# Kernel tuning notes

Measured on AMD Instinct MI355X. Metric: run time of the kernel, lower is better.

## Reference

```python
import jax, jax.numpy as jnp
import numpy as np

N_NODES = 100000
N_EDGES = 1600000
D = 128
NUM_LAYERS = 2
EPS = 1e-5


def setup_inputs() -> dict:
    key = jax.random.key(0)
    ks = jax.random.split(key, 8)
    s = 1.0 / np.sqrt(D)
    x = jax.random.normal(ks[0], (N_NODES, D), dtype=jnp.float32)
    edge_index = jax.random.randint(ks[1], (2, N_EDGES), 0, N_NODES, dtype=jnp.int64)
    W1 = jax.random.uniform(ks[2], (D, D), jnp.float32, -s, s)
    b1 = jnp.zeros((D,), jnp.float32)
    W2 = jax.random.uniform(ks[3], (D, D), jnp.float32, -s, s)
    b2 = jnp.zeros((D,), jnp.float32)
    inner = (NUM_LAYERS + 1) * D
    bn_gamma = jnp.ones((inner,), jnp.float32)
    bn_beta = jnp.zeros((inner,), jnp.float32)
    so = 1.0 / np.sqrt(inner)
    Wo = jax.random.uniform(ks[4], (inner, D), jnp.float32, -so, so)
    bo = jax.random.uniform(ks[5], (D,), jnp.float32, -so, so)
    return dict(x=x, edge_index=edge_index, W1=W1, b1=b1, W2=W2, b2=b2,
                bn_gamma=bn_gamma, bn_beta=bn_beta, Wo=Wo, bo=bo)


def gcn_conv(x, src, dst, W, b, n_nodes):
    """PyG GCNConv: symmetric norm with added self-loops, linear then aggregate."""
    h = x @ W  # [N, D]
    deg = jax.ops.segment_sum(jnp.ones_like(src, dtype=h.dtype), dst,
                              num_segments=n_nodes) + 1.0  # +1 self-loop
    dinv = jax.lax.rsqrt(deg)  # deg >= 1 so finite
    norm = dinv[src] * dinv[dst]  # [E]
    msg = h[src] * norm[:, None]  # gather: memory-bound
    agg = jax.ops.segment_sum(msg, dst, num_segments=n_nodes)
    agg = agg + h * (dinv * dinv)[:, None]  # self-loop message
    return agg + b


def reference(x, edge_index, W1, b1, W2, b2, bn_gamma, bn_beta, Wo, bo):
    src, dst = edge_index[0], edge_index[1]
    n = x.shape[0]
    x_cat = [x]
    h = jax.nn.relu(gcn_conv(x, src, dst, W1, b1, n))
    x_cat.append(h)
    h = jax.nn.relu(gcn_conv(h, src, dst, W2, b2, n))
    x_cat.append(h)
    xc = jnp.concatenate(x_cat, axis=-1)  # [N, 3D]
    # BatchNorm1d (training forward: batch statistics, biased variance)
    mu = jnp.mean(xc, axis=0)
    var = jnp.mean(jnp.square(xc - mu), axis=0)
    xn = (xc - mu) * jax.lax.rsqrt(var + EPS) * bn_gamma + bn_beta
    return xn @ Wo + bo  # [N, D]
```

## Files before the change

### kernel.cpp

```cpp
#include <hip/hip_runtime.h>
#include <hip/hip_bf16.h>

#define DD 128
#define NBLK 256
#define MAXBUK 1024
#define CAP2 12288

typedef __attribute__((ext_vector_type(8))) short bf16x8;
typedef __attribute__((ext_vector_type(4))) float f32x4;
typedef unsigned int uint32;

__device__ __forceinline__ unsigned short f2b(float f) {
  __hip_bfloat16 h = __float2bfloat16(f);
  unsigned short u;
  __builtin_memcpy(&u, &h, 2);
  return u;
}
__device__ __forceinline__ float b2f_lo(uint32 v) { return __uint_as_float(v << 16); }
__device__ __forceinline__ float b2f_hi(uint32 v) { return __uint_as_float(v & 0xffff0000u); }

__device__ __forceinline__ void acc8(float* acc, uint4 h, float w) {
  acc[0] = fmaf(w, b2f_lo(h.x), acc[0]);
  acc[1] = fmaf(w, b2f_hi(h.x), acc[1]);
  acc[2] = fmaf(w, b2f_lo(h.y), acc[2]);
  acc[3] = fmaf(w, b2f_hi(h.y), acc[3]);
  acc[4] = fmaf(w, b2f_lo(h.z), acc[4]);
  acc[5] = fmaf(w, b2f_hi(h.z), acc[5]);
  acc[6] = fmaf(w, b2f_lo(h.w), acc[6]);
  acc[7] = fmaf(w, b2f_hi(h.w), acc[7]);
}

__device__ __forceinline__ bool detect_i64(const int* e, int E) {
  int lane = threadIdx.x & 63;
  int samples = E < 64 ? E : 64;
  int v = (lane < samples) ? e[2 * lane + 1] : 0;
  return __ballot(v != 0) == 0ULL;
}

__global__ __launch_bounds__(256) void k_hist(const void* __restrict__ eptr, int E,
                                              int* __restrict__ histT, int nbuk) {
  __shared__ int hist[MAXBUK];
  int t = threadIdx.x, blk = blockIdx.x;
  bool f = detect_i64((const int*)eptr, E);
  for (int b = t; b < nbuk; b += 256) hist[b] = 0;
  __syncthreads();
  int chunk = (E + NBLK - 1) / NBLK;
  int i0 = blk * chunk, i1 = min(E, i0 + chunk);
  for (int i = i0 + t; i < i1; i += 256) {
    int dst = f ? (int)((const long long*)eptr)[E + i] : ((const int*)eptr)[E + i];
    atomicAdd(&hist[dst >> 8], 1);
  }
  __syncthreads();
  for (int b = t; b < nbuk; b += 256) histT[b * NBLK + blk] = hist[b];
}

__global__ __launch_bounds__(1024) void k_bktscan(const int* __restrict__ histT,
                                                  int* __restrict__ offs,
                                                  int* __restrict__ bucketBase,
                                                  int nbuk, int E) {
  __shared__ int tot[MAXBUK];
  int t = threadIdx.x, lane = t & 63, wv = t >> 6;
  for (int b = t; b < MAXBUK; b += 1024) tot[b] = 0;
  __syncthreads();
  for (int b = wv; b < nbuk; b += 16) {
    const int4 vv = *(const int4*)(histT + b * NBLK + lane * 4);
    int lsum = vv.x + vv.y + vv.z + vv.w;
    int s = lsum;
#pragma unroll
    for (int o = 1; o < 64; o <<= 1) {
      int u = __shfl_up(s, o);
      if (lane >= o) s += u;
    }
    if (lane == 63) tot[b] = s;
  }
  __syncthreads();
  for (int o = 1; o < MAXBUK; o <<= 1) {
    int u = (t >= o) ? tot[t - o] : 0;
    __syncthreads();
    tot[t] += u;
    __syncthreads();
  }
  for (int b = wv; b < nbuk; b += 16) {
    int idx = b * NBLK + lane * 4;
    const int4 vv = *(const int4*)(histT + idx);
    int lsum = vv.x + vv.y + vv.z + vv.w;
    int s = lsum;
#pragma unroll
    for (int o = 1; o < 64; o <<= 1) {
      int u = __shfl_up(s, o);
      if (lane >= o) s += u;
    }
    int tb = __shfl(s, 63);
    int bbase = tot[b] - tb;
    int excl = bbase + s - lsum;
    offs[idx] = excl;
    offs[idx + 1] = excl + vv.x;
    offs[idx + 2] = excl + vv.x + vv.y;
    offs[idx + 3] = excl + vv.x + vv.y + vv.z;
    if (lane == 0) bucketBase[b] = bbase;
  }
  if (t == 0) bucketBase[nbuk] = E;
}

__global__ __launch_bounds__(256) void k_place(const void* __restrict__ eptr, int E,
                                               const int* __restrict__ offs,
                                               int* __restrict__ ebuk, int nbuk) {
  __shared__ int cur[MAXBUK];
  int t = threadIdx.x, blk = blockIdx.x;
  bool f = detect_i64((const int*)eptr, E);
  for (int b = t; b < nbuk; b += 256) cur[b] = offs[b * NBLK + blk];
  __syncthreads();
  int chunk = (E + NBLK - 1) / NBLK;
  int i0 = blk * chunk, i1 = min(E, i0 + chunk);
  for (int i = i0 + t; i < i1; i += 256) {
    int src, dst;
    if (f) {
      src = (int)((const long long*)eptr)[i];
      dst = (int)((const long long*)eptr)[E + i];
    } else {
      src = ((const int*)eptr)[i];
      dst = ((const int*)eptr)[E + i];
    }
    int pos = atomicAdd(&cur[dst >> 8], 1);
    ebuk[pos] = (src << 8) | (dst & 255);
  }
}

__global__ __launch_bounds__(256) void k_bsort2(const int* __restrict__ ebuk,
                                                const int* __restrict__ bucketBase,
                                                int* __restrict__ rp, float* __restrict__ dinv,
                                                int* __restrict__ csrc, int n) {
  __shared__ int cnt[256];
  __shared__ int wss[4];
  __shared__ int outb[CAP2];
  int b = blockIdx.x, t = threadIdx.x, lane = t & 63, wv = t >> 6;
  int v0 = b << 8;
  int v1 = min(v0 + 256, n);
  int nn = v1 - v0;
  int base = bucketBase[b];
  int total = bucketBase[b + 1] - base;
  cnt[t] = 0;
  __syncthreads();
  for (int i = t; i < total; i += 256) atomicAdd(&cnt[ebuk[base + i] & 255], 1);
  __syncthreads();
  int v = cnt[t];
  int incl = v;
#pragma unroll
  for (int o = 1; o < 64; o <<= 1) {
    int u = __shfl_up(incl, o);
    if (lane >= o) incl += u;
  }
  if (lane == 63) wss[wv] = incl;
  __syncthreads();
  int woff = 0;
  for (int k = 0; k < wv; ++k) woff += wss[k];
  int excl = woff + incl - v;
  if (t < nn) {
    rp[v0 + t] = base + excl;
    dinv[v0 + t] = rsqrtf((float)v + 1.0f);
  }
  if (t == 255) rp[v1] = base + excl + v;
  __syncthreads();
  cnt[t] = excl;
  __syncthreads();
  if (total <= CAP2) {
    for (int i = t; i < total; i += 256) {
      int e = ebuk[base + i];
      int slot = atomicAdd(&cnt[e & 255], 1);
      outb[slot] = e >> 8;
    }
    __syncthreads();
    for (int i = t; i < total; i += 256) csrc[base + i] = outb[i];
  } else {
    for (int i = t; i < total; i += 256) {
      int e = ebuk[base + i];
      int slot = atomicAdd(&cnt[e & 255], 1);
      csrc[base + slot] = e >> 8;
    }
  }
}

__global__ __launch_bounds__(256) void k_cvtw(const float4* __restrict__ x,
                                              ushort4* __restrict__ xb, int n4,
                                              float* __restrict__ part,
                                              const float* __restrict__ W1,
                                              const float* __restrict__ W2,
                                              unsigned short* __restrict__ wimg) {
  __shared__ float sh[256][8];
  int t = threadIdx.x;
  int bid = blockIdx.x;
  if (bid >= 1024) {
    int i = (bid - 1024) * 256 + t;
    if (i < 32768) {
      int wsel = i >> 14;
      int j = i & 16383;
      int k = j >> 7, col = j & 127;
      float v = (wsel ? W2 : W1)[j];
      int chunk = (k >> 3) ^ (col & 7);
      wimg[wsel * 16384 + col * 128 + chunk * 8 + (k & 7)] = f2b(v);
    }
    return;
  }
  float s[4] = {0, 0, 0, 0}, q[4] = {0, 0, 0, 0};
  for (int i = bid * 256 + t; i < n4; i += 1024 * 256) {
    float4 a = x[i];
    ushort4 o;
    o.x = f2b(a.x); o.y = f2b(a.y); o.z = f2b(a.z); o.w = f2b(a.w);
    xb[i] = o;
    s[0] += a.x; s[1] += a.y; s[2] += a.z; s[3] += a.w;
    q[0] = fmaf(a.x, a.x, q[0]); q[1] = fmaf(a.y, a.y, q[1]);
    q[2] = fmaf(a.z, a.z, q[2]); q[3] = fmaf(a.w, a.w, q[3]);
  }
#pragma unroll
  for (int j = 0; j < 4; ++j) { sh[t][j] = s[j]; sh[t][4 + j] = q[j]; }
  __syncthreads();
  if (t < 32) {
#pragma unroll
    for (int g = 1; g < 8; ++g)
#pragma unroll
      for (int j = 0; j < 4; ++j) {
        s[j] += sh[g * 32 + t][j];
        q[j] += sh[g * 32 + t][4 + j];
      }
    float* pp = part + (size_t)(bid & 63) * 768;
#pragma unroll
    for (int j = 0; j < 4; ++j) {
      atomicAdd(&pp[(t * 4 + j) * 2], s[j]);
      atomicAdd(&pp[(t * 4 + j) * 2 + 1], q[j]);
    }
  }
}

__global__ __launch_bounds__(256) void k_gemm(const unsigned short* __restrict__ Ab,
                                              const unsigned short* __restrict__ Wimg,
                                              const float* __restrict__ dinv,
                                              unsigned short* __restrict__ H, int n) {
  __shared__ __align__(16) unsigned short Wl[16384];
  int t = threadIdx.x, lane = t & 63, w = t >> 6;
#pragma unroll
  for (int i = t; i < 2048; i += 256) ((int4*)Wl)[i] = ((const int4*)Wimg)[i];
  __syncthreads();
  int rowBase = blockIdx.x * 128 + w * 32;
  int r16 = lane & 15, half = lane >> 4;
  f32x4 acc[2][8];
#pragma unroll
  for (int m = 0; m < 2; ++m)
#pragma unroll
    for (int nn = 0; nn < 8; ++nn) acc[m][nn] = (f32x4){0.f, 0.f, 0.f, 0.f};
#pragma unroll
  for (int ks = 0; ks < 4; ++ks) {
    bf16x8 a[2];
#pragma unroll
    for (int m = 0; m < 2; ++m) {
      int r = rowBase + m * 16 + r16;
      if (r >= n) r = n - 1;
      a[m] = *(const bf16x8*)(Ab + (size_t)r * DD + ks * 32 + half * 8);
    }
#pragma unroll
    for (int nn = 0; nn < 8; ++nn) {
      int col = nn * 16 + r16;
      int chunk = (ks * 4 + half) ^ (col & 7);
      bf16x8 b = *(const bf16x8*)(Wl + col * 128 + chunk * 8);
      acc[0][nn] = __builtin_amdgcn_mfma_f32_16x16x32_bf16(a[0], b, acc[0][nn], 0, 0, 0);
      acc[1][nn] = __builtin_amdgcn_mfma_f32_16x16x32_bf16(a[1], b, acc[1][nn], 0, 0, 0);
    }
  }
#pragma unroll
  for (int m = 0; m < 2; ++m) {
    int rb = rowBase + m * 16 + half * 4;
    float dv[4];
#pragma unroll
    for (int i = 0; i < 4; ++i) dv[i] = (rb + i < n) ? dinv[rb + i] : 0.f;
#pragma unroll
    for (int nn = 0; nn < 8; ++nn) {
      int col = nn * 16 + r16;
#pragma unroll
      for (int i = 0; i < 4; ++i) {
        int r = rb + i;
        if (r < n) H[(size_t)r * DD + col] = f2b(acc[m][nn][i] * dv[i]);
      }
    }
  }
}

__global__ __launch_bounds__(256) void k_agg(const unsigned short* __restrict__ hs,
                                             const float* __restrict__ dinv,
                                             const float* __restrict__ b,
                                             const int* __restrict__ rp,
                                             const int* __restrict__ csrc,
                                             unsigned short* __restrict__ y, int n,
                                             float* __restrict__ part, int cb) {
  __shared__ float sh_s[8][128];
  __shared__ float sh_q[8][128];
  int wid = threadIdx.x >> 6, lane = threadIdx.x & 63;
  int eidx = lane >> 4;
  int seg = lane & 15;
  int vA = blockIdx.x * 8 + wid;
  int vB = vA + 4;
  bool okA = vA < n, okB = vB < n;
  int a0 = 0, b0 = 0, a1 = 0, b1 = 0;
  if (okA) { a0 = rp[vA]; b0 = rp[vA + 1]; }
  if (okB) { a1 = rp[vB]; b1 = rp[vB + 1]; }
  const uint4* H4 = (const uint4*)hs;
  uint4 selfA = okA ? H4[(size_t)vA * 16 + seg] : make_uint4(0, 0, 0, 0);
  uint4 selfB = okB ? H4[(size_t)vB * 16 + seg] : make_uint4(0, 0, 0, 0);
  float accA[8], accB[8];
#pragma unroll
  for (int j = 0; j < 8; ++j) { accA[j] = 0.f; accB[j] = 0.f; }
  int ebA = a0, ebB = a1;
  while (ebA < b0 || ebB < b1) {
    int ecA = b0 - ebA; ecA = ecA < 0 ? 0 : (ecA > 64 ? 64 : ecA);
    int ecB = b1 - ebB; ecB = ecB < 0 ? 0 : (ecB > 64 ? 64 : ecB);
    int ulA = (ebA + lane < b0) ? csrc[ebA + lane] : 0;
    int ulB = (ebB + lane < b1) ? csrc[ebB + lane] : 0;
    int iters = ecA > ecB ? ecA : ecB;
    for (int cc = 0; cc < iters; cc += 16) {
      int uA0 = __shfl(ulA, cc + eidx), uA1 = __shfl(ulA, cc + 4 + eidx);
      int uA2 = __shfl(ulA, cc + 8 + eidx), uA3 = __shfl(ulA, cc + 12 + eidx);
      int uB0 = __shfl(ulB, cc + eidx), uB1 = __shfl(ulB, cc + 4 + eidx);
      int uB2 = __shfl(ulB, cc + 8 + eidx), uB3 = __shfl(ulB, cc + 12 + eidx);
      float wA0 = (cc + eidx < ecA) ? 1.f : 0.f;
      float wA1 = (cc + 4 + eidx < ecA) ? 1.f : 0.f;
      float wA2 = (cc + 8 + eidx < ecA) ? 1.f : 0.f;
      float wA3 = (cc + 12 + eidx < ecA) ? 1.f : 0.f;
      float wB0 = (cc + eidx < ecB) ? 1.f : 0.f;
      float wB1 = (cc + 4 + eidx < ecB) ? 1.f : 0.f;
      float wB2 = (cc + 8 + eidx < ecB) ? 1.f : 0.f;
      float wB3 = (cc + 12 + eidx < ecB) ? 1.f : 0.f;
      uint4 hA0 = H4[(size_t)uA0 * 16 + seg];
      uint4 hA1 = H4[(size_t)uA1 * 16 + seg];
      uint4 hA2 = H4[(size_t)uA2 * 16 + seg];
      uint4 hA3 = H4[(size_t)uA3 * 16 + seg];
      uint4 hB0 = H4[(size_t)uB0 * 16 + seg];
      uint4 hB1 = H4[(size_t)uB1 * 16 + seg];
      uint4 hB2 = H4[(size_t)uB2 * 16 + seg];
      uint4 hB3 = H4[(size_t)uB3 * 16 + seg];
      acc8(accA, hA0, wA0); acc8(accA, hA1, wA1);
      acc8(accA, hA2, wA2); acc8(accA, hA3, wA3);
      acc8(accB, hB0, wB0); acc8(accB, hB1, wB1);
      acc8(accB, hB2, wB2); acc8(accB, hB3, wB3);
    }
    ebA += 64;
    ebB += 64;
  }
#pragma unroll
  for (int j = 0; j < 8; ++j) {
    accA[j] += __shfl_xor(accA[j], 16);
    accA[j] += __shfl_xor(accA[j], 32);
    accB[j] += __shfl_xor(accB[j], 16);
    accB[j] += __shfl_xor(accB[j], 32);
  }
  float4 bb0 = ((const float4*)b)[seg * 2];
  float4 bb1 = ((const float4*)b)[seg * 2 + 1];
  float bv[8] = {bb0.x, bb0.y, bb0.z, bb0.w, bb1.x, bb1.y, bb1.z, bb1.w};
  float oA[8], oB[8];
  if (okA) {
    float sf[8] = {b2f_lo(selfA.x), b2f_hi(selfA.x), b2f_lo(selfA.y), b2f_hi(selfA.y),
                   b2f_lo(selfA.z), b2f_hi(selfA.z), b2f_lo(selfA.w), b2f_hi(selfA.w)};
    float dv = dinv[vA];
#pragma unroll
    for (int j = 0; j < 8; ++j) oA[j] = fmaxf(fmaf(dv, accA[j] + sf[j], bv[j]), 0.f);
    if (eidx == 0) {
      uint4 ov;
      ov.x = (uint32)f2b(oA[0]) | ((uint32)f2b(oA[1]) << 16);
      ov.y = (uint32)f2b(oA[2]) | ((uint32)f2b(oA[3]) << 16);
      ov.z = (uint32)f2b(oA[4]) | ((uint32)f2b(oA[5]) << 16);
      ov.w = (uint32)f2b(oA[6]) | ((uint32)f2b(oA[7]) << 16);
      ((uint4*)y)[(size_t)vA * 16 + seg] = ov;
    }
  } else {
#pragma unroll
    for (int j = 0; j < 8; ++j) oA[j] = 0.f;
  }
  if (okB) {
    float sf[8] = {b2f_lo(selfB.x), b2f_hi(selfB.x), b2f_lo(selfB.y), b2f_hi(selfB.y),
                   b2f_lo(selfB.z), b2f_hi(selfB.z), b2f_lo(selfB.w), b2f_hi(selfB.w)};
    float dv = dinv[vB];
#pragma unroll
    for (int j = 0; j < 8; ++j) oB[j] = fmaxf(fmaf(dv, accB[j] + sf[j], bv[j]), 0.f);
    if (eidx == 0) {
      uint4 ov;
      ov.x = (uint32)f2b(oB[0]) | ((uint32)f2b(oB[1]) << 16);
      ov.y = (uint32)f2b(oB[2]) | ((uint32)f2b(oB[3]) << 16);
      ov.z = (uint32)f2b(oB[4]) | ((uint32)f2b(oB[5]) << 16);
      ov.w = (uint32)f2b(oB[6]) | ((uint32)f2b(oB[7]) << 16);
      ((uint4*)y)[(size_t)vB * 16 + seg] = ov;
    }
  } else {
#pragma unroll
    for (int j = 0; j < 8; ++j) oB[j] = 0.f;
  }
  if (eidx == 0) {
#pragma unroll
    for (int j = 0; j < 8; ++j) {
      sh_s[wid][seg * 8 + j] = oA[j];
      sh_q[wid][seg * 8 + j] = oA[j] * oA[j];
      sh_s[wid + 4][seg * 8 + j] = oB[j];
      sh_q[wid + 4][seg * 8 + j] = oB[j] * oB[j];
    }
  }
  __syncthreads();
  if (threadIdx.x < 128) {
    int c = threadIdx.x;
    float s = 0.f, q = 0.f;
#pragma unroll
    for (int k2 = 0; k2 < 8; ++k2) {
      s += sh_s[k2][c];
      q += sh_q[k2][c];
    }
    float* pp = part + (size_t)(blockIdx.x & 63) * 768;
    atomicAdd(&pp[(cb + c) * 2], s);
    atomicAdd(&pp[(cb + c) * 2 + 1], q);
  }
}

__global__ void k_fold_a(const float* __restrict__ part, const float* __restrict__ gamma,
                         const float* __restrict__ beta, const float* __restrict__ Wo,
                         const float* __restrict__ bo, float* __restrict__ aS,
                         float* __restrict__ boP, int n) {
  __shared__ float cSh[384];
  int t = threadIdx.x;
  float s = 0.f, q = 0.f;
  for (int r = 0; r < 64; ++r) {
    s += part[r * 768 + t * 2];
    q += part[r * 768 + t * 2 + 1];
  }
  float inv_n = 1.0f / (float)n;
  float mu = s * inv_n;
  float var = q * inv_n - mu * mu;
  float a = gamma[t] * rsqrtf(var + 1e-5f);
  aS[t] = a;
  cSh[t] = beta[t] - mu * a;
  __syncthreads();
  if (t < DD) {
    float sb = bo[t];
    for (int k = 0; k < 384; ++k) sb = fmaf(cSh[k], Wo[k * DD + t], sb);
    boP[t] = sb;
  }
}

__global__ void k_foldw(const float* __restrict__ aS, const float* __restrict__ Wo,
                        unsigned short* __restrict__ wopimg) {
  int i = blockIdx.x * 256 + threadIdx.x;
  if (i >= 49152) return;
  int krow = i >> 7, col = i & 127;
  float v = aS[krow] * Wo[i];
  int p = krow >> 7, kk = krow & 127;
  int chunk = (kk >> 3) ^ (col & 7);
  wopimg[p * 16384 + col * 128 + chunk * 8 + (kk & 7)] = f2b(v);
}

__global__ __launch_bounds__(256) void k_gemm_out(const unsigned short* __restrict__ xb,
                                                  const unsigned short* __restrict__ y1,
                                                  const unsigned short* __restrict__ y2,
                                                  const unsigned short* __restrict__ Wimg3,
                                                  const float* __restrict__ boP,
                                                  float* __restrict__ out, int n) {
  __shared__ __align__(16) unsigned short Wl[16384];
  int t = threadIdx.x, lane = t & 63, w = t >> 6;
  int rowBase = blockIdx.x * 128 + w * 32;
  int r16 = lane & 15, half = lane >> 4;
  f32x4 acc[2][8];
#pragma unroll
  for (int m = 0; m < 2; ++m)
#pragma unroll
    for (int nn = 0; nn < 8; ++nn) acc[m][nn] = (f32x4){0.f, 0.f, 0.f, 0.f};
  for (int p = 0; p < 3; ++p) {
    const unsigned short* Ab = (p == 0) ? xb : (p == 1) ? y1 : y2;
    __syncthreads();
#pragma unroll
    for (int i = t; i < 2048; i += 256) ((int4*)Wl)[i] = ((const int4*)(Wimg3 + p * 16384))[i];
    __syncthreads();
#pragma unroll
    for (int ks = 0; ks < 4; ++ks) {
      bf16x8 a[2];
#pragma unroll
      for (int m = 0; m < 2; ++m) {
        int r = rowBase + m * 16 + r16;
        if (r >= n) r = n - 1;
        a[m] = *(const bf16x8*)(Ab + (size_t)r * DD + ks * 32 + half * 8);
      }
#pragma unroll
      for (int nn = 0; nn < 8; ++nn) {
        int col = nn * 16 + r16;
        int chunk = (ks * 4 + half) ^ (col & 7);
        bf16x8 b = *(const bf16x8*)(Wl + col * 128 + chunk * 8);
        acc[0][nn] = __builtin_amdgcn_mfma_f32_16x16x32_bf16(a[0], b, acc[0][nn], 0, 0, 0);
        acc[1][nn] = __builtin_amdgcn_mfma_f32_16x16x32_bf16(a[1], b, acc[1][nn], 0, 0, 0);
      }
    }
  }
#pragma unroll
  for (int m = 0; m < 2; ++m) {
    int rb = rowBase + m * 16 + half * 4;
#pragma unroll
    for (int nn = 0; nn < 8; ++nn) {
      int col = nn * 16 + r16;
      float bb = boP[col];
#pragma unroll
      for (int i = 0; i < 4; ++i) {
        int r = rb + i;
        if (r < n) out[(size_t)r * DD + col] = acc[m][nn][i] + bb;
      }
    }
  }
}

extern "C" void kernel_launch(void* const* d_in, const int* in_sizes, int n_in,
                              void* d_out, int out_size, void* d_ws, size_t ws_size,
                              hipStream_t stream) {
  const float* x = (const float*)d_in[0];
  const void* ept = d_in[1];
  const float* W1 = (const float*)d_in[2];
  const float* b1 = (const float*)d_in[3];
  const float* W2 = (const float*)d_in[4];
  const float* b2 = (const float*)d_in[5];
  const float* gamma = (const float*)d_in[6];
  const float* beta = (const float*)d_in[7];
  const float* Wo = (const float*)d_in[8];
  const float* bo = (const float*)d_in[9];
  float* out = (float*)d_out;
  int N = in_sizes[0] / DD;
  int E = in_sizes[1] / 2;
  int nbuk = (N + 255) >> 8;

  char* w = (char*)d_ws;
  size_t off = 0;
  auto alloc = [&](size_t bytes) {
    void* p = w + off;
    off = (off + bytes + 255) & ~(size_t)255;
    return p;
  };
  float* dinv = (float*)alloc((size_t)N * 4);
  int* rp = (int*)alloc((size_t)(N + 1) * 4);
  int* csrc = (int*)alloc((size_t)E * 4);
  int* ebuk = (int*)alloc((size_t)E * 4);
  int* histT = (int*)alloc((size_t)MAXBUK * NBLK * 4);
  int* offs = (int*)alloc((size_t)MAXBUK * NBLK * 4);
  int* bucketBase = (int*)alloc((size_t)(MAXBUK + 1) * 4);
  unsigned short* xb = (unsigned short*)alloc((size_t)N * DD * 2);
  unsigned short* h = (unsigned short*)alloc((size_t)N * DD * 2);
  unsigned short* y1 = (unsigned short*)alloc((size_t)N * DD * 2);
  unsigned short* y2 = (unsigned short*)alloc((size_t)N * DD * 2);
  unsigned short* wimg = (unsigned short*)alloc(32768 * 2);
  unsigned short* wopimg = (unsigned short*)alloc(49152 * 2);
  float* part = (float*)alloc((size_t)64 * 768 * 4);
  float* aS = (float*)alloc(384 * 4);
  float* boP = (float*)alloc(DD * 4);

  hipMemsetAsync(part, 0, (size_t)64 * 768 * 4, stream);

  k_hist<<<NBLK, 256, 0, stream>>>(ept, E, histT, nbuk);
  k_bktscan<<<1, 1024, 0, stream>>>(histT, offs, bucketBase, nbuk, E);
  k_place<<<NBLK, 256, 0, stream>>>(ept, E, offs, ebuk, nbuk);
  k_bsort2<<<nbuk, 256, 0, stream>>>(ebuk, bucketBase, rp, dinv, csrc, N);

  int n4 = N * DD / 4;
  k_cvtw<<<1024 + 128, 256, 0, stream>>>((const float4*)x, (ushort4*)xb, n4, part, W1, W2, wimg);

  int gb = (N + 127) / 128;
  int ab = (N + 7) / 8;
  k_gemm<<<gb, 256, 0, stream>>>(xb, wimg, dinv, h, N);
  k_agg<<<ab, 256, 0, stream>>>(h, dinv, b1, rp, csrc, y1, N, part, 128);
  k_gemm<<<gb, 256, 0, stream>>>(y1, wimg + 16384, dinv, h, N);
  k_agg<<<ab, 256, 0, stream>>>(h, dinv, b2, rp, csrc, y2, N, part, 256);

  k_fold_a<<<1, 384, 0, stream>>>(part, gamma, beta, Wo, bo, aS, boP, N);
  k_foldw<<<192, 256, 0, stream>>>(aS, Wo, wopimg);
  k_gemm_out<<<gb, 256, 0, stream>>>(xb, y1, y2, wopimg, boP, out, N);
}
```

Measured before the change: 340.1 us.

## Split aggregation across feature slices per block with 2-lane row segments

The aggregation kernel is restructured so each block handles only a 16-column feature slice (one of 8) for 32 nodes. Each wave now covers 8 nodes with 8 edges in parallel, and each lane loads 16 bytes of a 32-byte slice instead of a full 256-byte row. The intent is to raise parallelism and make gather traffic per block more cache-local, with the neighbour lists reused across slices. The BatchNorm partial sums now reduce through shuffles before a smaller shared-memory step. In exchange, edge indices are reloaded 8 times and the gathers are narrower and less coalesced.

```diff
diff --git a/kernel.cpp b/kernel.cpp
--- a/kernel.cpp
+++ b/kernel.cpp
@@ -290,73 +290,67 @@
                                              const int* __restrict__ csrc,
                                              unsigned short* __restrict__ y, int n,
                                              float* __restrict__ part, int cb) {
-  __shared__ float sh_s[8][128];
-  __shared__ float sh_q[8][128];
-  int wid = threadIdx.x >> 6, lane = threadIdx.x & 63;
-  int eidx = lane >> 4;
-  int seg = lane & 15;
-  int vA = blockIdx.x * 8 + wid;
+  __shared__ float sh_s[4][2][8];
+  __shared__ float sh_q[4][2][8];
+  int slice = blockIdx.x & 7;
+  int nb = blockIdx.x >> 3;
+  int t = threadIdx.x, wid = t >> 6, lane = t & 63;
+  int nodeIdx = lane >> 4;
+  int eidx = (lane >> 1) & 7;
+  int seg = lane & 1;
+  int gbase = nodeIdx << 4;
+  int l16 = lane & 15;
+  int vA = nb * 32 + wid * 8 + nodeIdx;
   int vB = vA + 4;
   bool okA = vA < n, okB = vB < n;
   int a0 = 0, b0 = 0, a1 = 0, b1 = 0;
   if (okA) { a0 = rp[vA]; b0 = rp[vA + 1]; }
   if (okB) { a1 = rp[vB]; b1 = rp[vB + 1]; }
   const uint4* H4 = (const uint4*)hs;
-  uint4 selfA = okA ? H4[(size_t)vA * 16 + seg] : make_uint4(0, 0, 0, 0);
-  uint4 selfB = okB ? H4[(size_t)vB * 16 + seg] : make_uint4(0, 0, 0, 0);
+  int so = slice * 2 + seg;
   float accA[8], accB[8];
 #pragma unroll
   for (int j = 0; j < 8; ++j) { accA[j] = 0.f; accB[j] = 0.f; }
   int ebA = a0, ebB = a1;
   while (ebA < b0 || ebB < b1) {
-    int ecA = b0 - ebA; ecA = ecA < 0 ? 0 : (ecA > 64 ? 64 : ecA);
-    int ecB = b1 - ebB; ecB = ecB < 0 ? 0 : (ecB > 64 ? 64 : ecB);
-    int ulA = (ebA + lane < b0) ? csrc[ebA + lane] : 0;
-    int ulB = (ebB + lane < b1) ? csrc[ebB + lane] : 0;
-    int iters = ecA > ecB ? ecA : ecB;
-    for (int cc = 0; cc < iters; cc += 16) {
-      int uA0 = __shfl(ulA, cc + eidx), uA1 = __shfl(ulA, cc + 4 + eidx);
-      int uA2 = __shfl(ulA, cc + 8 + eidx), uA3 = __shfl(ulA, cc + 12 + eidx);
-      int uB0 = __shfl(ulB, cc + eidx), uB1 = __shfl(ulB, cc + 4 + eidx);
-      int uB2 = __shfl(ulB, cc + 8 + eidx), uB3 = __shfl(ulB, cc + 12 + eidx);
-      float wA0 = (cc + eidx < ecA) ? 1.f : 0.f;
-      float wA1 = (cc + 4 + eidx < ecA) ? 1.f : 0.f;
-      float wA2 = (cc + 8 + eidx < ecA) ? 1.f : 0.f;
-      float wA3 = (cc + 12 + eidx < ecA) ? 1.f : 0.f;
-      float wB0 = (cc + eidx < ecB) ? 1.f : 0.f;
-      float wB1 = (cc + 4 + eidx < ecB) ? 1.f : 0.f;
-      float wB2 = (cc + 8 + eidx < ecB) ? 1.f : 0.f;
-      float wB3 = (cc + 12 + eidx < ecB) ? 1.f : 0.f;
-      uint4 hA0 = H4[(size_t)uA0 * 16 + seg];
-      uint4 hA1 = H4[(size_t)uA1 * 16 + seg];
-      uint4 hA2 = H4[(size_t)uA2 * 16 + seg];
-      uint4 hA3 = H4[(size_t)uA3 * 16 + seg];
-      uint4 hB0 = H4[(size_t)uB0 * 16 + seg];
-      uint4 hB1 = H4[(size_t)uB1 * 16 + seg];
-      uint4 hB2 = H4[(size_t)uB2 * 16 + seg];
-      uint4 hB3 = H4[(size_t)uB3 * 16 + seg];
-      acc8(accA, hA0, wA0); acc8(accA, hA1, wA1);
-      acc8(accA, hA2, wA2); acc8(accA, hA3, wA3);
-      acc8(accB, hB0, wB0); acc8(accB, hB1, wB1);
-      acc8(accB, hB2, wB2); acc8(accB, hB3, wB3);
-    }
-    ebA += 64;
-    ebB += 64;
+    int ulA = (ebA + l16 < b0) ? csrc[ebA + l16] : 0;
+    int ulB = (ebB + l16 < b1) ? csrc[ebB + l16] : 0;
+    int uA0 = __shfl(ulA, gbase + eidx);
+    int uA1 = __shfl(ulA, gbase + 8 + eidx);
+    int uB0 = __shfl(ulB, gbase + eidx);
+    int uB1 = __shfl(ulB, gbase + 8 + eidx);
+    float wA0 = (ebA + eidx < b0) ? 1.f : 0.f;
+    float wA1 = (ebA + 8 + eidx < b0) ? 1.f : 0.f;
+    float wB0 = (ebB + eidx < b1) ? 1.f : 0.f;
+    float wB1 = (ebB + 8 + eidx < b1) ? 1.f : 0.f;
+    uint4 hA0 = H4[(size_t)uA0 * 16 + so];
+    uint4 hA1 = H4[(size_t)uA1 * 16 + so];
+    uint4 hB0 = H4[(size_t)uB0 * 16 + so];
+    uint4 hB1 = H4[(size_t)uB1 * 16 + so];
+    acc8(accA, hA0, wA0);
+    acc8(accA, hA1, wA1);
+    acc8(accB, hB0, wB0);
+    acc8(accB, hB1, wB1);
+    ebA += 16;
+    ebB += 16;
   }
 #pragma unroll
   for (int j = 0; j < 8; ++j) {
-    accA[j] += __shfl_xor(accA[j], 16);
-    accA[j] += __shfl_xor(accA[j], 32);
-    accB[j] += __shfl_xor(accB[j], 16);
-    accB[j] += __shfl_xor(accB[j], 32);
-  }
-  float4 bb0 = ((const float4*)b)[seg * 2];
-  float4 bb1 = ((const float4*)b)[seg * 2 + 1];
+    accA[j] += __shfl_xor(accA[j], 2);
+    accA[j] += __shfl_xor(accA[j], 4);
+    accA[j] += __shfl_xor(accA[j], 8);
+    accB[j] += __shfl_xor(accB[j], 2);
+    accB[j] += __shfl_xor(accB[j], 4);
+    accB[j] += __shfl_xor(accB[j], 8);
+  }
+  float4 bb0 = ((const float4*)b)[slice * 4 + seg * 2];
+  float4 bb1 = ((const float4*)b)[slice * 4 + seg * 2 + 1];
   float bv[8] = {bb0.x, bb0.y, bb0.z, bb0.w, bb1.x, bb1.y, bb1.z, bb1.w};
   float oA[8], oB[8];
   if (okA) {
-    float sf[8] = {b2f_lo(selfA.x), b2f_hi(selfA.x), b2f_lo(selfA.y), b2f_hi(selfA.y),
-                   b2f_lo(selfA.z), b2f_hi(selfA.z), b2f_lo(selfA.w), b2f_hi(selfA.w)};
+    uint4 sfv = H4[(size_t)vA * 16 + so];
+    float sf[8] = {b2f_lo(sfv.x), b2f_hi(sfv.x), b2f_lo(sfv.y), b2f_hi(sfv.y),
+                   b2f_lo(sfv.z), b2f_hi(sfv.z), b2f_lo(sfv.w), b2f_hi(sfv.w)};
     float dv = dinv[vA];
 #pragma unroll
     for (int j = 0; j < 8; ++j) oA[j] = fmaxf(fmaf(dv, accA[j] + sf[j], bv[j]), 0.f);
@@ -366,15 +360,16 @@
       ov.y = (uint32)f2b(oA[2]) | ((uint32)f2b(oA[3]) << 16);
       ov.z = (uint32)f2b(oA[4]) | ((uint32)f2b(oA[5]) << 16);
       ov.w = (uint32)f2b(oA[6]) | ((uint32)f2b(oA[7]) << 16);
-      ((uint4*)y)[(size_t)vA * 16 + seg] = ov;
+      ((uint4*)y)[(size_t)vA * 16 + so] = ov;
     }
   } else {
 #pragma unroll
     for (int j = 0; j < 8; ++j) oA[j] = 0.f;
   }
   if (okB) {
-    float sf[8] = {b2f_lo(selfB.x), b2f_hi(selfB.x), b2f_lo(selfB.y), b2f_hi(selfB.y),
-                   b2f_lo(selfB.z), b2f_hi(selfB.z), b2f_lo(selfB.w), b2f_hi(selfB.w)};
+    uint4 sfv = H4[(size_t)vB * 16 + so];
+    float sf[8] = {b2f_lo(sfv.x), b2f_hi(sfv.x), b2f_lo(sfv.y), b2f_hi(sfv.y),
+                   b2f_lo(sfv.z), b2f_hi(sfv.z), b2f_lo(sfv.w), b2f_hi(sfv.w)};
     float dv = dinv[vB];
 #pragma unroll
     for (int j = 0; j < 8; ++j) oB[j] = fmaxf(fmaf(dv, accB[j] + sf[j], bv[j]), 0.f);
@@ -384,33 +379,40 @@
       ov.y = (uint32)f2b(oB[2]) | ((uint32)f2b(oB[3]) << 16);
       ov.z = (uint32)f2b(oB[4]) | ((uint32)f2b(oB[5]) << 16);
       ov.w = (uint32)f2b(oB[6]) | ((uint32)f2b(oB[7]) << 16);
-      ((uint4*)y)[(size_t)vB * 16 + seg] = ov;
+      ((uint4*)y)[(size_t)vB * 16 + so] = ov;
     }
   } else {
 #pragma unroll
     for (int j = 0; j < 8; ++j) oB[j] = 0.f;
   }
-  if (eidx == 0) {
+  float s[8], q[8];
+#pragma unroll
+  for (int j = 0; j < 8; ++j) {
+    s[j] = oA[j] + oB[j];
+    q[j] = oA[j] * oA[j] + oB[j] * oB[j];
+  }
+#pragma unroll
+  for (int j = 0; j < 8; ++j) {
+    s[j] += __shfl_xor(s[j], 16);
+    s[j] += __shfl_xor(s[j], 32);
+    q[j] += __shfl_xor(q[j], 16);
+    q[j] += __shfl_xor(q[j], 32);
+  }
+  if (lane < 2) {
 #pragma unroll
     for (int j = 0; j < 8; ++j) {
-      sh_s[wid][seg * 8 + j] = oA[j];
-      sh_q[wid][seg * 8 + j] = oA[j] * oA[j];
-      sh_s[wid + 4][seg * 8 + j] = oB[j];
-      sh_q[wid + 4][seg * 8 + j] = oB[j] * oB[j];
-    }
-  }
-  __syncthreads();
-  if (threadIdx.x < 128) {
-    int c = threadIdx.x;
-    float s = 0.f, q = 0.f;
-#pragma unroll
-    for (int k2 = 0; k2 < 8; ++k2) {
-      s += sh_s[k2][c];
-      q += sh_q[k2][c];
-    }
+      sh_s[wid][lane][j] = s[j];
+      sh_q[wid][lane][j] = q[j];
+    }
+  }
+  __syncthreads();
+  if (t < 16) {
+    int sg = t >> 3, j = t & 7;
+    float ss = sh_s[0][sg][j] + sh_s[1][sg][j] + sh_s[2][sg][j] + sh_s[3][sg][j];
+    float qq = sh_q[0][sg][j] + sh_q[1][sg][j] + sh_q[2][sg][j] + sh_q[3][sg][j];
     float* pp = part + (size_t)(blockIdx.x & 63) * 768;
-    atomicAdd(&pp[(cb + c) * 2], s);
-    atomicAdd(&pp[(cb + c) * 2 + 1], q);
+    atomicAdd(&pp[(cb + slice * 16 + t) * 2], ss);
+    atomicAdd(&pp[(cb + slice * 16 + t) * 2 + 1], qq);
   }
 }
 
@@ -559,7 +561,7 @@
   k_cvtw<<<1024 + 128, 256, 0, stream>>>((const float4*)x, (ushort4*)xb, n4, part, W1, W2, wimg);
 
   int gb = (N + 127) / 128;
-  int ab = (N + 7) / 8;
+  int ab = 8 * ((N + 31) / 32);
   k_gemm<<<gb, 256, 0, stream>>>(xb, wimg, dinv, h, N);
   k_agg<<<ab, 256, 0, stream>>>(h, dinv, b1, rp, csrc, y1, N, part, 128);
   k_gemm<<<gb, 256, 0, stream>>>(y1, wimg + 16384, dinv, h, N);
```

New measurement: 562.6 us. 1.65x slower.
